# Kernel optimization log

Measured on AMD Instinct MI355X. Metric: run time of the kernel, lower is better.

The kernel has to match this reference:

```python
import jax, jax.numpy as jnp
import numpy as np

N_KEYS, PER_KEY = 8, 6
NUM_CONCEPTS = N_KEYS * PER_KEY  # 48
NUM_CLASS = 7
D_VIT, D = 768, 512
LOGIT_SCALE = 100.0


def adaptive_avg_pool_matrix(L_in: int, L_out: int) -> np.ndarray:
    """Linear operator replicating torch AdaptiveAvgPool1d: out[i] = mean(x[start_i:end_i])."""
    M = np.zeros((L_in, L_out), dtype=np.float32)
    for i in range(L_out):
        s = (i * L_in) // L_out
        e = -(((-(i + 1)) * L_in) // L_out)  # ceil((i+1)*L_in/L_out)
        M[s:e, i] = 1.0 / (e - s)
    return M


def setup_inputs() -> dict:
    key = jax.random.key(0)
    ks = jax.random.split(key, 12)
    feats = jax.random.normal(ks[0], (12, 32, 197, D_VIT), dtype=jnp.float32)
    # frozen text-side concept embeddings (CLIP text feats are ~unit norm, 512-d)
    ce = jax.random.normal(ks[1], (NUM_CONCEPTS, D), dtype=jnp.float32)
    concept_embeds = ce / jnp.linalg.norm(ce, axis=-1, keepdims=True)
    sc = 1.0 / np.sqrt(D_VIT)
    W_lin = jax.random.normal(ks[2], (D, D_VIT), dtype=jnp.float32) * sc
    b_lin = jnp.zeros((D,), dtype=jnp.float32)
    W_proj = jax.random.normal(ks[3], (D, D_VIT), dtype=jnp.float32) * sc
    scg = 1.0 / np.sqrt(3 * D)
    W_gate = jax.random.normal(ks[4], (D, 3 * D), dtype=jnp.float32) * scg
    b_gate = jnp.zeros((D,), dtype=jnp.float32)
    scu = 1.0 / np.sqrt(2 * D)
    W_upd = jax.random.normal(ks[5], (D, 2 * D), dtype=jnp.float32) * scu
    b_upd = jnp.zeros((D,), dtype=jnp.float32)
    W_cls = jax.random.normal(ks[6], (NUM_CLASS, NUM_CONCEPTS), dtype=jnp.float32) / np.sqrt(NUM_CONCEPTS)
    b_cls = jnp.zeros((NUM_CLASS,), dtype=jnp.float32)
    return {
        'feats': feats, 'concept_embeds': concept_embeds,
        'W_lin': W_lin, 'b_lin': b_lin, 'W_proj': W_proj,
        'W_gate': W_gate, 'b_gate': b_gate, 'W_upd': W_upd, 'b_upd': b_upd,
        'W_cls': W_cls, 'b_cls': b_cls,
    }


def _forward(feats, concept_embeds, W_lin, b_lin, W_proj, W_gate, b_gate, W_upd, b_upd, W_cls, b_cls):
    L, B, S, _ = feats.shape
    M = jnp.asarray(adaptive_avg_pool_matrix(S - 1, NUM_CONCEPTS))  # [196, 48]
    q0 = jnp.broadcast_to(concept_embeds[None], (B, NUM_CONCEPTS, D))

    def step(q, f):  # f: [B, 197, 768]
        cls_tok = f[:, :1, :]                                  # [B,1,768]
        pooled = jnp.einsum('bjd,ji->bid', f[:, 1:, :], M)     # [B,48,768]
        vt = jnp.concatenate([cls_tok, pooled], axis=1) @ W_lin.T + b_lin  # [B,49,512]
        attn = jax.nn.softmax(jnp.einsum('bqd,bvd->bqv', q, vt), axis=-1)
        fuse = jnp.einsum('bqv,bvd->bqd', attn, vt)            # [B,48,512]
        cls_ctx = jnp.broadcast_to(cls_tok @ W_proj.T, q.shape)
        gate = jax.nn.sigmoid(jnp.concatenate([fuse, q, cls_ctx], -1) @ W_gate.T + b_gate)
        upd = jnp.tanh(jnp.concatenate([fuse, q], -1) @ W_upd.T + b_upd)
        return gate * q + (1.0 - gate) * upd, fuse

    _, trace = jax.lax.scan(step, q0, feats)                   # trace: [12,B,48,512]

    last = trace[-1]
    vision_semantic = last / jnp.maximum(jnp.linalg.norm(last, axis=-1, keepdims=True), 1e-12)
    vs = vision_semantic.reshape(B, N_KEYS, PER_KEY, D)
    anchors = concept_embeds.reshape(N_KEYS, PER_KEY, D)
    image_logits = (LOGIT_SCALE * jnp.einsum('bkpd,kqd->bkpq', vs, anchors).mean(axis=2)).reshape(B, NUM_CONCEPTS)
    cls_logits = image_logits @ W_cls.T + b_cls
    diffs = trace[1:] - jax.lax.stop_gradient(trace[:-1])
    loss_consistency = jnp.sum(jnp.mean(diffs * diffs, axis=(1, 2, 3)))
    return cls_logits, image_logits, loss_consistency


def reference(feats, concept_embeds, W_lin, b_lin, W_proj, W_gate, b_gate, W_upd, b_upd, W_cls, b_cls):
    return _forward(feats, concept_embeds, W_lin, b_lin, W_proj, W_gate, b_gate, W_upd, b_upd, W_cls, b_cls)
```

## Files before the change

### kernel.cpp

```cpp
#include <hip/hip_runtime.h>
#include <hip/hip_bf16.h>

#define LL 12
#define BB 32
#define SS 197
#define DV 768
#define DD 512
#define CC 48
#define VV 49
#define LOSS_DEN 786432.0f

typedef unsigned short u16;
typedef unsigned int u32;
using bf16x8 = __attribute__((ext_vector_type(8))) __bf16;
using f32x4 = __attribute__((ext_vector_type(4))) float;
using u16x8 = __attribute__((ext_vector_type(8))) u16;
using u16x4 = __attribute__((ext_vector_type(4))) u16;

__device__ __forceinline__ u16 bf16h(float x) {
    u32 u = __builtin_bit_cast(u32, x);
    return (u16)((u + 0x7FFFu + ((u >> 16) & 1u)) >> 16);
}
__device__ __forceinline__ float bf2f(u16 h) {
    u32 u = ((u32)h) << 16;
    return __builtin_bit_cast(float, u);
}
__device__ __forceinline__ f32x4 mfma16(bf16x8 a, bf16x8 b, f32x4 c) {
    return __builtin_amdgcn_mfma_f32_16x16x32_bf16(a, b, c, 0, 0, 0);
}
__device__ __forceinline__ void gl_lds16(const void* g, void* s) {
    __builtin_amdgcn_global_load_lds((const __attribute__((address_space(1))) u32*)g,
                                     (__attribute__((address_space(3))) u32*)s, 16, 0, 0);
}

#define NLW (512 * 768)
#define NGW (512 * 1536)
#define NUW (512 * 1024)
#define POOL2_BLKS (LL * BB * 2)
#define WSPLIT4_BLKS ((NLW + NGW + NUW) / 1024)
#define INITQ8_BLKS ((BB * CC * DD) / 2048)

__global__ __launch_bounds__(256) void mega_pre(const float* __restrict__ feats,
                                                const float* __restrict__ Wl,
                                                const float* __restrict__ Wg,
                                                const float* __restrict__ Wu,
                                                const float* __restrict__ ce,
                                                u16* __restrict__ Xh, u16* __restrict__ Xl,
                                                u16* Wlh, u16* Wll, u16* Wgh, u16* Wgl,
                                                u16* Wuh, u16* Wul,
                                                u16* __restrict__ qh, u16* __restrict__ ql,
                                                float* __restrict__ loss) {
    int bid = blockIdx.x;
    int t = threadIdx.x;
    if (bid < POOL2_BLKS) {
        if (t >= 192) return;
        int lb = bid >> 1, half = bid & 1;
        const float4* fb = (const float4*)(feats + (size_t)lb * SS * DV);
        size_t xbase = (size_t)lb * VV * DV + 4 * t;
        if (half == 0) {
            float4 c = fb[t];
            float cv[4] = {c.x, c.y, c.z, c.w};
            u16x4 hh, ll2;
#pragma unroll
            for (int j = 0; j < 4; ++j) {
                u16 h = bf16h(cv[j]);
                hh[j] = h;
                ll2[j] = bf16h(cv[j] - bf2f(h));
            }
            *(u16x4*)(Xh + xbase) = hh;
            *(u16x4*)(Xl + xbase) = ll2;
        }
        int ib0 = half * 24, ib1 = ib0 + 24;
        for (int i = ib0; i < ib1; ++i) {
            int s = (i * 196) / 48;
            int e = ((i + 1) * 196 + 47) / 48;
            float4 acc = {0.f, 0.f, 0.f, 0.f};
            for (int j = s; j < e; ++j) {
                float4 v = fb[(size_t)(1 + j) * 192 + t];
                acc.x += v.x; acc.y += v.y; acc.z += v.z; acc.w += v.w;
            }
            float inv = 1.0f / (float)(e - s);
            float av[4] = {acc.x * inv, acc.y * inv, acc.z * inv, acc.w * inv};
            u16x4 hh, ll2;
#pragma unroll
            for (int j = 0; j < 4; ++j) {
                u16 h = bf16h(av[j]);
                hh[j] = h;
                ll2[j] = bf16h(av[j] - bf2f(h));
            }
            size_t o = xbase + (size_t)(1 + i) * DV;
            *(u16x4*)(Xh + o) = hh;
            *(u16x4*)(Xl + o) = ll2;
        }
    } else if (bid < POOL2_BLKS + WSPLIT4_BLKS) {
        int i = ((bid - POOL2_BLKS) * 256 + t) * 4;
        float4 v;
        u16 *ph, *pl;
        int j;
        if (i < NLW) { v = *(const float4*)(Wl + i); ph = Wlh; pl = Wll; j = i; }
        else if (i < NLW + NGW) { j = i - NLW; v = *(const float4*)(Wg + j); ph = Wgh; pl = Wgl; }
        else { j = i - NLW - NGW; v = *(const float4*)(Wu + j); ph = Wuh; pl = Wul; }
        float vv[4] = {v.x, v.y, v.z, v.w};
        u16x4 hh, ll2;
#pragma unroll
        for (int k = 0; k < 4; ++k) {
            u16 h = bf16h(vv[k]);
            hh[k] = h;
            ll2[k] = bf16h(vv[k] - bf2f(h));
        }
        *(u16x4*)(ph + j) = hh;
        *(u16x4*)(pl + j) = ll2;
    } else {
        int i8 = ((bid - POOL2_BLKS - WSPLIT4_BLKS) * 256 + t) * 8;
        int src = i8 % (CC * DD);
        float4 a = *(const float4*)(ce + src);
        float4 b2 = *(const float4*)(ce + src + 4);
        float vv[8] = {a.x, a.y, a.z, a.w, b2.x, b2.y, b2.z, b2.w};
        u16x8 hh, ll2;
#pragma unroll
        for (int k = 0; k < 8; ++k) {
            u16 h = bf16h(vv[k]);
            hh[k] = h;
            ll2[k] = bf16h(vv[k] - bf2f(h));
        }
        *(u16x8*)(qh + i8) = hh;
        *(u16x8*)(ql + i8) = ll2;
        if (i8 == 0) loss[0] = 0.0f;
    }
}

__global__ __launch_bounds__(256) void gemm_f32(const float* __restrict__ A, int lda,
                                                const float* __restrict__ W, int wstride, int K,
                                                const float* __restrict__ bias,
                                                float* __restrict__ Cout) {
    __shared__ float As[32][65];
    __shared__ float Bs[32][65];
    int t = threadIdx.x;
    int m0 = blockIdx.x * 64;
    int n0 = blockIdx.y * 64;
    int r = t >> 2;
    int kc = (t & 3) * 8;
    int tx = t & 15, ty = t >> 4;
    float acc[4][4] = {};
    for (int k0 = 0; k0 < K; k0 += 32) {
        const float4* pa = (const float4*)(A + (size_t)(m0 + r) * lda + k0 + kc);
        float4 a0 = pa[0], a1 = pa[1];
        const float4* pw = (const float4*)(W + (size_t)(n0 + r) * wstride + k0 + kc);
        float4 w0 = pw[0], w1 = pw[1];
        As[kc + 0][r] = a0.x; As[kc + 1][r] = a0.y; As[kc + 2][r] = a0.z; As[kc + 3][r] = a0.w;
        As[kc + 4][r] = a1.x; As[kc + 5][r] = a1.y; As[kc + 6][r] = a1.z; As[kc + 7][r] = a1.w;
        Bs[kc + 0][r] = w0.x; Bs[kc + 1][r] = w0.y; Bs[kc + 2][r] = w0.z; Bs[kc + 3][r] = w0.w;
        Bs[kc + 4][r] = w1.x; Bs[kc + 5][r] = w1.y; Bs[kc + 6][r] = w1.z; Bs[kc + 7][r] = w1.w;
        __syncthreads();
#pragma unroll
        for (int kk = 0; kk < 32; ++kk) {
            float a[4], b[4];
#pragma unroll
            for (int i = 0; i < 4; ++i) { a[i] = As[kk][ty * 4 + i]; b[i] = Bs[kk][tx * 4 + i]; }
#pragma unroll
            for (int i = 0; i < 4; ++i)
#pragma unroll
                for (int j = 0; j < 4; ++j) acc[i][j] += a[i] * b[j];
        }
        __syncthreads();
    }
#pragma unroll
    for (int i = 0; i < 4; ++i) {
        int m = m0 + ty * 4 + i;
#pragma unroll
        for (int j = 0; j < 4; ++j) {
            int n = n0 + tx * 4 + j;
            Cout[(size_t)m * DD + n] = acc[i][j] + (bias ? bias[n] : 0.0f);
        }
    }
}

__global__ __launch_bounds__(256, 2) void vt_gemm(const u16* __restrict__ Xh, const u16* __restrict__ Xl,
                                                  const u16* __restrict__ Wh, const u16* __restrict__ Wl,
                                                  const float* __restrict__ bias,
                                                  u16* __restrict__ vthp, u16* __restrict__ vtlp) {
    __shared__ u16 sm[24576];
    int tid = threadIdx.x;
    int w = tid >> 6, l = tid & 63, lr = l & 15, ls = l >> 4;
    int i = blockIdx.x, m, n;
    if (i < 1152) { int a = i >> 6, r2 = i & 63; m = 8 * a + (r2 & 7); n = r2 >> 3; }
    else { int j = i - 1152; m = 144 + (j >> 3); n = j & 7; }
    int m0 = m * 128, n0 = n * 64;
    f32x4 acc[2][4];
#pragma unroll
    for (int ii = 0; ii < 2; ++ii)
#pragma unroll
        for (int j = 0; j < 4; ++j) acc[ii][j] = f32x4{0.f, 0.f, 0.f, 0.f};

    auto stage = [&](u16* dst, int k0) {
#pragma unroll
        for (int is = 0; is < 6; ++is) {
            int q = is * 256 + tid;
            const u16* src;
            int off;
            if (is < 2)      { int qr = q;        int row = qr >> 2, sl = qr & 3; src = Xh + (size_t)(m0 + row) * DV + k0 + ((sl ^ ((row >> 1) & 3)) << 3); off = qr * 8; }
            else if (is < 4) { int qr = q - 512;  int row = qr >> 2, sl = qr & 3; src = Xl + (size_t)(m0 + row) * DV + k0 + ((sl ^ ((row >> 1) & 3)) << 3); off = 4096 + qr * 8; }
            else if (is < 5) { int qr = q - 1024; int row = qr >> 2, sl = qr & 3; src = Wh + (size_t)(n0 + row) * DV + k0 + ((sl ^ ((row >> 1) & 3)) << 3); off = 8192 + qr * 8; }
            else             { int qr = q - 1280; int row = qr >> 2, sl = qr & 3; src = Wl + (size_t)(n0 + row) * DV + k0 + ((sl ^ ((row >> 1) & 3)) << 3); off = 10240 + qr * 8; }
            gl_lds16(src, dst + off);
        }
    };

    stage(sm, 0);
    __syncthreads();
    for (int t = 0; t < 24; ++t) {
        u16* cur = sm + ((t & 1) ? 12288 : 0);
        u16* nxt = sm + ((t & 1) ? 0 : 12288);
        if (t + 1 < 24) stage(nxt, (t + 1) * 32);
        bf16x8 ah[2], al2[2], bh[4], bl2[4];
#pragma unroll
        for (int rf = 0; rf < 2; ++rf) {
            int row = 32 * w + 16 * rf + lr;
            int ro = row * 32 + ((ls ^ ((row >> 1) & 3)) << 3);
            ah[rf] = *(const bf16x8*)(cur + ro);
            al2[rf] = *(const bf16x8*)(cur + 4096 + ro);
        }
#pragma unroll
        for (int cf = 0; cf < 4; ++cf) {
            int nn = 16 * cf + lr;
            int no = nn * 32 + ((ls ^ ((nn >> 1) & 3)) << 3);
            bh[cf] = *(const bf16x8*)(cur + 8192 + no);
            bl2[cf] = *(const bf16x8*)(cur + 10240 + no);
        }
#pragma unroll
        for (int rf = 0; rf < 2; ++rf)
#pragma unroll
            for (int cf = 0; cf < 4; ++cf) {
                acc[rf][cf] = mfma16(ah[rf], bh[cf], acc[rf][cf]);
                acc[rf][cf] = mfma16(ah[rf], bl2[cf], acc[rf][cf]);
                acc[rf][cf] = mfma16(al2[rf], bh[cf], acc[rf][cf]);
            }
        __syncthreads();
    }
#pragma unroll
    for (int rf = 0; rf < 2; ++rf)
#pragma unroll
        for (int cf = 0; cf < 4; ++cf)
#pragma unroll
            for (int r = 0; r < 4; ++r) {
                int row = m0 + 32 * w + 16 * rf + 4 * ls + r;
                int col = n0 + 16 * cf + lr;
                float v = acc[rf][cf][r] + bias[col];
                size_t o = (size_t)row * DD + col;
                u16 hh = bf16h(v);
                vthp[o] = hh;
                vtlp[o] = bf16h(v - bf2f(hh));
            }
}

__device__ __forceinline__ void gemm32x64(u16* sm, const u16* Ah, const u16* Al,
                                          const u16* Wgh, const u16* Wgl,
                                          const u16* Wuh, const u16* Wul,
                                          int m0, int n0, int colOff, int tid,
                                          f32x4 accg[2], f32x4 accu[2]) {
    int w = tid >> 6, lane = tid & 63, lr = lane & 15, ls = lane >> 4;
    auto stage = [&](u16* buf, int k0) {
        {
            int j = tid, row = j >> 3, sl = j & 7;
            int ko = k0 + ((sl ^ (row & 7)) << 3);
            gl_lds16(Ah + (size_t)(m0 + row) * DD + ko, buf + j * 8);
            gl_lds16(Al + (size_t)(m0 + row) * DD + ko, buf + 2048 + j * 8);
        }
#pragma unroll
        for (int i2 = 0; i2 < 8; ++i2) {
            int aidx = tid + 256 * i2;
            int arr = aidx >> 9, j = aidx & 511;
            int row = j >> 3, sl = j & 7;
            int ko = colOff + k0 + ((sl ^ (row & 7)) << 3);
            const u16* src;
            if (arr == 0) src = Wgh + (size_t)(n0 + row) * 1536 + ko;
            else if (arr == 1) src = Wgl + (size_t)(n0 + row) * 1536 + ko;
            else if (arr == 2) src = Wuh + (size_t)(n0 + row) * 1024 + ko;
            else src = Wul + (size_t)(n0 + row) * 1024 + ko;
            gl_lds16(src, buf + 4096 + arr * 4096 + j * 8);
        }
    };
    stage(sm, 0);
    __syncthreads();
    for (int t = 0; t < 8; ++t) {
        u16* cur = sm + (t & 1) * 20480;
        if (t + 1 < 8) stage(sm + ((t + 1) & 1) * 20480, (t + 1) * 64);
#pragma unroll
        for (int ks = 0; ks < 2; ++ks) {
            int slot = ks * 4 + ls;
            int n = 16 * w + lr;
            int bo = n * 64 + ((slot ^ (n & 7)) << 3);
            bf16x8 gh8 = *(const bf16x8*)(cur + 4096 + bo);
            bf16x8 gl8 = *(const bf16x8*)(cur + 8192 + bo);
            bf16x8 uh8 = *(const bf16x8*)(cur + 12288 + bo);
            bf16x8 ul8 = *(const bf16x8*)(cur + 16384 + bo);
#pragma unroll
            for (int rf = 0; rf < 2; ++rf) {
                int r = 16 * rf + lr;
                int ao = r * 64 + ((slot ^ (r & 7)) << 3);
                bf16x8 ah8 = *(const bf16x8*)(cur + ao);
                bf16x8 al8 = *(const bf16x8*)(cur + 2048 + ao);
                accg[rf] = mfma16(ah8, gh8, accg[rf]);
                accg[rf] = mfma16(ah8, gl8, accg[rf]);
                accg[rf] = mfma16(al8, gh8, accg[rf]);
                accu[rf] = mfma16(ah8, uh8, accu[rf]);
                accu[rf] = mfma16(ah8, ul8, accu[rf]);
                accu[rf] = mfma16(al8, uh8, accu[rf]);
            }
        }
        __syncthreads();
    }
}

__global__ __launch_bounds__(256, 2) void attn_qpart(
    const u16* __restrict__ qh, const u16* __restrict__ ql,
    const u16* __restrict__ vthL, const u16* __restrict__ vtlL,
    float* __restrict__ fcur, const float* __restrict__ fprev,
    u16* __restrict__ fh, u16* __restrict__ fl,
    float* __restrict__ loss, int do_loss,
    const u16* __restrict__ Wgh, const u16* __restrict__ Wgl,
    const u16* __restrict__ Wuh, const u16* __restrict__ Wul,
    float* __restrict__ qg, float* __restrict__ qu) {
    __shared__ u16 sm[40960];
    int tid = threadIdx.x;
    if (blockIdx.x < 192) {
        int wgid = blockIdx.x * 4 + (tid >> 6);
        int lane = tid & 63;
        int b = wgid / 24;
        int r0 = b * CC + (wgid % 24) * 2;
        size_t o0 = (size_t)r0 * DD + lane * 8;
        u16x8 h0 = *(const u16x8*)(qh + o0), g0 = *(const u16x8*)(ql + o0);
        u16x8 h1 = *(const u16x8*)(qh + o0 + DD), g1 = *(const u16x8*)(ql + o0 + DD);
        float q0v[8], q1v[8];
#pragma unroll
        for (int j = 0; j < 8; ++j) {
            q0v[j] = bf2f(h0[j]) + bf2f(g0[j]);
            q1v[j] = bf2f(h1[j]) + bf2f(g1[j]);
        }
        const u16* vh = vthL + (size_t)b * VV * DD + lane * 8;
        const u16* vl = vtlL + (size_t)b * VV * DD + lane * 8;
        float m0 = -3e38f, m1 = -3e38f, s0 = 0.f, s1 = 0.f;
        float a0[8] = {}, a1[8] = {};
        for (int v = 0; v < VV; ++v) {
            u16x8 rh = *(const u16x8*)(vh + v * DD);
            u16x8 rl = *(const u16x8*)(vl + v * DD);
            float rv[8];
#pragma unroll
            for (int j = 0; j < 8; ++j) rv[j] = bf2f(rh[j]) + bf2f(rl[j]);
            float p0 = 0.f, p1 = 0.f;
#pragma unroll
            for (int j = 0; j < 8; ++j) { p0 += q0v[j] * rv[j]; p1 += q1v[j] * rv[j]; }
#pragma unroll
            for (int off = 32; off > 0; off >>= 1) { p0 += __shfl_xor(p0, off); p1 += __shfl_xor(p1, off); }
            float nm0 = fmaxf(m0, p0);
            float sc0 = __expf(m0 - nm0), w0 = __expf(p0 - nm0);
            s0 = s0 * sc0 + w0;
            float nm1 = fmaxf(m1, p1);
            float sc1 = __expf(m1 - nm1), w1 = __expf(p1 - nm1);
            s1 = s1 * sc1 + w1;
#pragma unroll
            for (int j = 0; j < 8; ++j) {
                a0[j] = a0[j] * sc0 + w0 * rv[j];
                a1[j] = a1[j] * sc1 + w1 * rv[j];
            }
            m0 = nm0;
            m1 = nm1;
        }
        float inv0 = 1.0f / s0, inv1 = 1.0f / s1;
        float d2 = 0.f;
        float f0v[8], f1v[8];
        u16x8 oh0, ol0, oh1, ol1;
#pragma unroll
        for (int j = 0; j < 8; ++j) {
            float f = a0[j] * inv0;
            f0v[j] = f;
            u16 hh = bf16h(f);
            oh0[j] = hh;
            ol0[j] = bf16h(f - bf2f(hh));
            float f2 = a1[j] * inv1;
            f1v[j] = f2;
            u16 h2 = bf16h(f2);
            oh1[j] = h2;
            ol1[j] = bf16h(f2 - bf2f(h2));
        }
        *(float4*)(fcur + o0) = float4{f0v[0], f0v[1], f0v[2], f0v[3]};
        *(float4*)(fcur + o0 + 4) = float4{f0v[4], f0v[5], f0v[6], f0v[7]};
        *(float4*)(fcur + o0 + DD) = float4{f1v[0], f1v[1], f1v[2], f1v[3]};
        *(float4*)(fcur + o0 + DD + 4) = float4{f1v[4], f1v[5], f1v[6], f1v[7]};
        *(u16x8*)(fh + o0) = oh0;
        *(u16x8*)(fl + o0) = ol0;
        *(u16x8*)(fh + o0 + DD) = oh1;
        *(u16x8*)(fl + o0 + DD) = ol1;
        if (do_loss) {
#pragma unroll
            for (int j = 0; j < 8; ++j) {
                float d = f0v[j] - fprev[o0 + j];
                d2 += d * d;
                float e = f1v[j] - fprev[o0 + DD + j];
                d2 += e * e;
            }
#pragma unroll
            for (int off = 32; off > 0; off >>= 1) d2 += __shfl_xor(d2, off);
            if (lane == 0) atomicAdd(loss, d2);
        }
    } else {
        int tb = blockIdx.x - 192;
        int m0 = (tb >> 3) * 32, n0 = (tb & 7) * 64;
        f32x4 accg[2], accu[2];
#pragma unroll
        for (int i = 0; i < 2; ++i) { accg[i] = f32x4{0.f, 0.f, 0.f, 0.f}; accu[i] = f32x4{0.f, 0.f, 0.f, 0.f}; }
        gemm32x64(sm, qh, ql, Wgh, Wgl, Wuh, Wul, m0, n0, 512, tid, accg, accu);
        int w = tid >> 6, lane = tid & 63, lr = lane & 15, ls = lane >> 4;
#pragma unroll
        for (int rf = 0; rf < 2; ++rf)
#pragma unroll
            for (int r = 0; r < 4; ++r) {
                int row = m0 + 16 * rf + 4 * ls + r;
                int col = n0 + 16 * w + lr;
                size_t o = (size_t)row * DD + col;
                qg[o] = accg[rf][r];
                qu[o] = accu[rf][r];
            }
    }
}

__global__ __launch_bounds__(256, 2) void fusepart(
    const u16* __restrict__ fhp, const u16* __restrict__ flp,
    const u16* __restrict__ qhp, const u16* __restrict__ qlp,
    const u16* __restrict__ Wgh, const u16* __restrict__ Wgl,
    const u16* __restrict__ Wuh, const u16* __restrict__ Wul,
    const float* __restrict__ qg, const float* __restrict__ qu,
    const float* __restrict__ CgL, const float* __restrict__ bu,
    u16* __restrict__ qoh, u16* __restrict__ qol) {
    __shared__ u16 sm[40960];
    int tid = threadIdx.x;
    int m0 = (blockIdx.x >> 3) * 32, n0 = (blockIdx.x & 7) * 64;
    f32x4 accg[2], accu[2];
#pragma unroll
    for (int i = 0; i < 2; ++i) { accg[i] = f32x4{0.f, 0.f, 0.f, 0.f}; accu[i] = f32x4{0.f, 0.f, 0.f, 0.f}; }
    gemm32x64(sm, fhp, flp, Wgh, Wgl, Wuh, Wul, m0, n0, 0, tid, accg, accu);
    int w = tid >> 6, lane = tid & 63, lr = lane & 15, ls = lane >> 4;
#pragma unroll
    for (int rf = 0; rf < 2; ++rf)
#pragma unroll
        for (int r = 0; r < 4; ++r) {
            int row = m0 + 16 * rf + 4 * ls + r;
            int col = n0 + 16 * w + lr;
            int b = row / CC;
            size_t o = (size_t)row * DD + col;
            float gpre = accg[rf][r] + qg[o] + CgL[(size_t)b * DD + col];
            float upre = accu[rf][r] + qu[o] + bu[col];
            float g = 1.0f / (1.0f + __expf(-gpre));
            float u = tanhf(upre);
            float qv = bf2f(qhp[o]) + bf2f(qlp[o]);
            float qo = g * qv + (1.0f - g) * u;
            u16 hh = bf16h(qo);
            qoh[o] = hh;
            qol[o] = bf16h(qo - bf2f(hh));
        }
}

__global__ __launch_bounds__(256) void final_kernel(const float* __restrict__ fuse_last,
                                                    const float* __restrict__ ce,
                                                    const float* __restrict__ W_cls,
                                                    const float* __restrict__ b_cls,
                                                    const float* __restrict__ loss_acc,
                                                    float* __restrict__ out) {
    int b = blockIdx.x;
    int t = threadIdx.x;
    int w = t >> 6, lane = t & 63;
    __shared__ float invn[CC];
    __shared__ float img[CC];
    const float* fb = fuse_last + (size_t)b * CC * DD;
    for (int c = w; c < CC; c += 4) {
        const float* fr = fb + (size_t)c * DD + lane * 8;
        float4 a0 = *(const float4*)fr;
        float4 a1 = *(const float4*)(fr + 4);
        float ss = a0.x * a0.x + a0.y * a0.y + a0.z * a0.z + a0.w * a0.w +
                   a1.x * a1.x + a1.y * a1.y + a1.z * a1.z + a1.w * a1.w;
#pragma unroll
        for (int off = 32; off > 0; off >>= 1) ss += __shfl_xor(ss, off);
        if (lane == 0) invn[c] = 1.0f / fmaxf(sqrtf(ss), 1e-12f);
    }
    __syncthreads();
    for (int g = w; g < CC; g += 4) {
        int k = g / 6;
        const float* ar = ce + (size_t)g * DD + lane * 8;
        float4 c0 = *(const float4*)ar;
        float4 c1 = *(const float4*)(ar + 4);
        float av[8] = {c0.x, c0.y, c0.z, c0.w, c1.x, c1.y, c1.z, c1.w};
        float accp = 0.0f;
        for (int p = 0; p < 6; ++p) {
            int row = k * 6 + p;
            const float* fr = fb + (size_t)row * DD + lane * 8;
            float4 f0 = *(const float4*)fr;
            float4 f1 = *(const float4*)(fr + 4);
            float fv[8] = {f0.x, f0.y, f0.z, f0.w, f1.x, f1.y, f1.z, f1.w};
            float d = 0.0f;
#pragma unroll
            for (int j = 0; j < 8; ++j) d += fv[j] * av[j];
            accp += d * invn[row];
        }
#pragma unroll
        for (int off = 32; off > 0; off >>= 1) accp += __shfl_xor(accp, off);
        if (lane == 0) img[g] = accp * (100.0f / 6.0f);
    }
    __syncthreads();
    if (t < CC) out[BB * 7 + b * CC + t] = img[t];
    if (t < 7) {
        float sacc = b_cls[t];
        for (int c = 0; c < CC; ++c) sacc += img[c] * W_cls[t * CC + c];
        out[b * 7 + t] = sacc;
    }
    if (b == 0 && t == 0) out[BB * 7 + BB * CC] = loss_acc[0] * (1.0f / LOSS_DEN);
}

extern "C" void kernel_launch(void* const* d_in, const int* in_sizes, int n_in,
                              void* d_out, int out_size, void* d_ws, size_t ws_size,
                              hipStream_t stream) {
    const float* feats = (const float*)d_in[0];
    const float* ce = (const float*)d_in[1];
    const float* W_lin = (const float*)d_in[2];
    const float* b_lin = (const float*)d_in[3];
    const float* W_proj = (const float*)d_in[4];
    const float* W_gate = (const float*)d_in[5];
    const float* b_gate = (const float*)d_in[6];
    const float* W_upd = (const float*)d_in[7];
    const float* b_upd = (const float*)d_in[8];
    const float* W_cls = (const float*)d_in[9];
    const float* b_cls = (const float*)d_in[10];
    float* out = (float*)d_out;

    char* base = (char*)d_ws;
    size_t off = 0;
    auto alloc = [&](size_t bytes) -> char* {
        char* r = base + off;
        off += (bytes + 255) & ~(size_t)255;
        return r;
    };
    u16* Xh = (u16*)alloc((size_t)LL * BB * VV * DV * 2);
    u16* Xl = (u16*)alloc((size_t)LL * BB * VV * DV * 2);
    u16* vth = (u16*)alloc((size_t)LL * BB * VV * DD * 2);
    u16* vtl = (u16*)alloc((size_t)LL * BB * VV * DD * 2);
    float* ctx = (float*)alloc((size_t)LL * BB * DD * 4);
    float* Cg = (float*)alloc((size_t)LL * BB * DD * 4);
    float* fbuf0 = (float*)alloc((size_t)BB * CC * DD * 4);
    float* fbuf1 = (float*)alloc((size_t)BB * CC * DD * 4);
    float* qg = (float*)alloc((size_t)BB * CC * DD * 4);
    float* qu = (float*)alloc((size_t)BB * CC * DD * 4);
    float* loss = (float*)alloc(256);
    u16* Wlh = (u16*)alloc((size_t)NLW * 2);
    u16* Wll = (u16*)alloc((size_t)NLW * 2);
    u16* Wgh = (u16*)alloc((size_t)NGW * 2);
    u16* Wgl = (u16*)alloc((size_t)NGW * 2);
    u16* Wuh = (u16*)alloc((size_t)NUW * 2);
    u16* Wul = (u16*)alloc((size_t)NUW * 2);
    u16* fh = (u16*)alloc((size_t)BB * CC * DD * 2);
    u16* fl = (u16*)alloc((size_t)BB * CC * DD * 2);
    u16* qah = (u16*)alloc((size_t)BB * CC * DD * 2);
    u16* qal = (u16*)alloc((size_t)BB * CC * DD * 2);
    u16* qbh = (u16*)alloc((size_t)BB * CC * DD * 2);
    u16* qbl = (u16*)alloc((size_t)BB * CC * DD * 2);
    u16* qph[2] = {qah, qbh};
    u16* qpl[2] = {qal, qbl};

    mega_pre<<<POOL2_BLKS + WSPLIT4_BLKS + INITQ8_BLKS, 256, 0, stream>>>(
        feats, W_lin, W_gate, W_upd, ce, Xh, Xl, Wlh, Wll, Wgh, Wgl, Wuh, Wul, qah, qal, loss);
    {
        dim3 g(LL * BB / 64, DD / 64);
        gemm_f32<<<g, 256, 0, stream>>>(feats, SS * DV, W_proj, DV, DV, nullptr, ctx);
        gemm_f32<<<g, 256, 0, stream>>>(ctx, DD, W_gate + 1024, 1536, DD, b_gate, Cg);
    }
    vt_gemm<<<1176, 256, 0, stream>>>(Xh, Xl, Wlh, Wll, b_lin, vth, vtl);

    int qc = 0;
    for (int l = 0; l < LL; ++l) {
        float* fcur = (l & 1) ? fbuf1 : fbuf0;
        const float* fprev = (l & 1) ? fbuf0 : fbuf1;
        int grid = (l < LL - 1) ? 576 : 192;
        attn_qpart<<<grid, 256, 0, stream>>>(qph[qc], qpl[qc],
                                             vth + (size_t)l * BB * VV * DD, vtl + (size_t)l * BB * VV * DD,
                                             fcur, fprev, fh, fl, loss, l > 0 ? 1 : 0,
                                             Wgh, Wgl, Wuh, Wul, qg, qu);
        if (l < LL - 1) {
            fusepart<<<384, 256, 0, stream>>>(fh, fl, qph[qc], qpl[qc],
                                              Wgh, Wgl, Wuh, Wul, qg, qu,
                                              Cg + (size_t)l * BB * DD, b_upd,
                                              qph[qc ^ 1], qpl[qc ^ 1]);
            qc ^= 1;
        }
    }

    final_kernel<<<BB, 256, 0, stream>>>((LL - 1) & 1 ? fbuf1 : fbuf0, ce, W_cls, b_cls, loss, out);
}
```

Measured before the change: 940.3 us.

## Drop weight low-part MFMAs in gate/update GEMMs and fold ctx GEMMs into existing kernels

Removes the bf16 low-part of W_gate/W_upd from the split-precision GEMM, halving weight staging in LDS and cutting MFMAs per step from six to four. The smaller shared buffer lets launch bounds rise to three blocks per CU. The two fp32 ctx/Cg GEMMs are folded into mega_pre and vt_gemm as extra blocks, eliminating two launches. The trade is lower precision in the weight product (roughly bf16 weights times a split-precision activation), which may affect accuracy.

```diff
diff --git a/kernel.cpp b/kernel.cpp
--- a/kernel.cpp
+++ b/kernel.cpp
@@ -36,108 +36,18 @@
 #define NLW (512 * 768)
 #define NGW (512 * 1536)
 #define NUW (512 * 1024)
+#define CTX_BLKS 48
 #define POOL2_BLKS (LL * BB * 2)
 #define WSPLIT4_BLKS ((NLW + NGW + NUW) / 1024)
 #define INITQ8_BLKS ((BB * CC * DD) / 2048)
 
-__global__ __launch_bounds__(256) void mega_pre(const float* __restrict__ feats,
-                                                const float* __restrict__ Wl,
-                                                const float* __restrict__ Wg,
-                                                const float* __restrict__ Wu,
-                                                const float* __restrict__ ce,
-                                                u16* __restrict__ Xh, u16* __restrict__ Xl,
-                                                u16* Wlh, u16* Wll, u16* Wgh, u16* Wgl,
-                                                u16* Wuh, u16* Wul,
-                                                u16* __restrict__ qh, u16* __restrict__ ql,
-                                                float* __restrict__ loss) {
-    int bid = blockIdx.x;
-    int t = threadIdx.x;
-    if (bid < POOL2_BLKS) {
-        if (t >= 192) return;
-        int lb = bid >> 1, half = bid & 1;
-        const float4* fb = (const float4*)(feats + (size_t)lb * SS * DV);
-        size_t xbase = (size_t)lb * VV * DV + 4 * t;
-        if (half == 0) {
-            float4 c = fb[t];
-            float cv[4] = {c.x, c.y, c.z, c.w};
-            u16x4 hh, ll2;
-#pragma unroll
-            for (int j = 0; j < 4; ++j) {
-                u16 h = bf16h(cv[j]);
-                hh[j] = h;
-                ll2[j] = bf16h(cv[j] - bf2f(h));
-            }
-            *(u16x4*)(Xh + xbase) = hh;
-            *(u16x4*)(Xl + xbase) = ll2;
-        }
-        int ib0 = half * 24, ib1 = ib0 + 24;
-        for (int i = ib0; i < ib1; ++i) {
-            int s = (i * 196) / 48;
-            int e = ((i + 1) * 196 + 47) / 48;
-            float4 acc = {0.f, 0.f, 0.f, 0.f};
-            for (int j = s; j < e; ++j) {
-                float4 v = fb[(size_t)(1 + j) * 192 + t];
-                acc.x += v.x; acc.y += v.y; acc.z += v.z; acc.w += v.w;
-            }
-            float inv = 1.0f / (float)(e - s);
-            float av[4] = {acc.x * inv, acc.y * inv, acc.z * inv, acc.w * inv};
-            u16x4 hh, ll2;
-#pragma unroll
-            for (int j = 0; j < 4; ++j) {
-                u16 h = bf16h(av[j]);
-                hh[j] = h;
-                ll2[j] = bf16h(av[j] - bf2f(h));
-            }
-            size_t o = xbase + (size_t)(1 + i) * DV;
-            *(u16x4*)(Xh + o) = hh;
-            *(u16x4*)(Xl + o) = ll2;
-        }
-    } else if (bid < POOL2_BLKS + WSPLIT4_BLKS) {
-        int i = ((bid - POOL2_BLKS) * 256 + t) * 4;
-        float4 v;
-        u16 *ph, *pl;
-        int j;
-        if (i < NLW) { v = *(const float4*)(Wl + i); ph = Wlh; pl = Wll; j = i; }
-        else if (i < NLW + NGW) { j = i - NLW; v = *(const float4*)(Wg + j); ph = Wgh; pl = Wgl; }
-        else { j = i - NLW - NGW; v = *(const float4*)(Wu + j); ph = Wuh; pl = Wul; }
-        float vv[4] = {v.x, v.y, v.z, v.w};
-        u16x4 hh, ll2;
-#pragma unroll
-        for (int k = 0; k < 4; ++k) {
-            u16 h = bf16h(vv[k]);
-            hh[k] = h;
-            ll2[k] = bf16h(vv[k] - bf2f(h));
-        }
-        *(u16x4*)(ph + j) = hh;
-        *(u16x4*)(pl + j) = ll2;
-    } else {
-        int i8 = ((bid - POOL2_BLKS - WSPLIT4_BLKS) * 256 + t) * 8;
-        int src = i8 % (CC * DD);
-        float4 a = *(const float4*)(ce + src);
-        float4 b2 = *(const float4*)(ce + src + 4);
-        float vv[8] = {a.x, a.y, a.z, a.w, b2.x, b2.y, b2.z, b2.w};
-        u16x8 hh, ll2;
-#pragma unroll
-        for (int k = 0; k < 8; ++k) {
-            u16 h = bf16h(vv[k]);
-            hh[k] = h;
-            ll2[k] = bf16h(vv[k] - bf2f(h));
-        }
-        *(u16x8*)(qh + i8) = hh;
-        *(u16x8*)(ql + i8) = ll2;
-        if (i8 == 0) loss[0] = 0.0f;
-    }
-}
-
-__global__ __launch_bounds__(256) void gemm_f32(const float* __restrict__ A, int lda,
-                                                const float* __restrict__ W, int wstride, int K,
-                                                const float* __restrict__ bias,
-                                                float* __restrict__ Cout) {
-    __shared__ float As[32][65];
-    __shared__ float Bs[32][65];
-    int t = threadIdx.x;
-    int m0 = blockIdx.x * 64;
-    int n0 = blockIdx.y * 64;
+__device__ __forceinline__ void gemm_f32_tile(const float* __restrict__ A, int lda,
+                                              const float* __restrict__ W, int wstride, int K,
+                                              const float* __restrict__ bias,
+                                              float* __restrict__ Cout,
+                                              int m0, int n0, int t, float* AsB, float* BsB) {
+    float (*As)[65] = (float(*)[65])AsB;
+    float (*Bs)[65] = (float(*)[65])BsB;
     int r = t >> 2;
     int kc = (t & 3) * 8;
     int tx = t & 15, ty = t >> 4;
@@ -175,12 +85,118 @@
     }
 }
 
+__global__ __launch_bounds__(256) void mega_pre(const float* __restrict__ feats,
+                                                const float* __restrict__ Wl,
+                                                const float* __restrict__ Wg,
+                                                const float* __restrict__ Wu,
+                                                const float* __restrict__ Wp,
+                                                const float* __restrict__ ce,
+                                                u16* __restrict__ Xh, u16* __restrict__ Xl,
+                                                u16* Wlh, u16* Wll, u16* Wgh, u16* Wgl,
+                                                u16* Wuh, u16* Wul,
+                                                u16* __restrict__ qh, u16* __restrict__ ql,
+                                                float* __restrict__ loss,
+                                                float* __restrict__ ctx) {
+    __shared__ float smf[2 * 32 * 65];
+    int bid = blockIdx.x;
+    int t = threadIdx.x;
+    if (bid < CTX_BLKS) {
+        gemm_f32_tile(feats, SS * DV, Wp, DV, DV, nullptr, ctx,
+                      (bid >> 3) * 64, (bid & 7) * 64, t, smf, smf + 32 * 65);
+    } else if (bid < CTX_BLKS + POOL2_BLKS) {
+        if (t >= 192) return;
+        int pb = bid - CTX_BLKS;
+        int lb = pb >> 1, half = pb & 1;
+        const float4* fb = (const float4*)(feats + (size_t)lb * SS * DV);
+        size_t xbase = (size_t)lb * VV * DV + 4 * t;
+        if (half == 0) {
+            float4 c = fb[t];
+            float cv[4] = {c.x, c.y, c.z, c.w};
+            u16x4 hh, ll2;
+#pragma unroll
+            for (int j = 0; j < 4; ++j) {
+                u16 h = bf16h(cv[j]);
+                hh[j] = h;
+                ll2[j] = bf16h(cv[j] - bf2f(h));
+            }
+            *(u16x4*)(Xh + xbase) = hh;
+            *(u16x4*)(Xl + xbase) = ll2;
+        }
+        int ib0 = half * 24, ib1 = ib0 + 24;
+        for (int i = ib0; i < ib1; ++i) {
+            int s = (i * 196) / 48;
+            int e = ((i + 1) * 196 + 47) / 48;
+            float4 acc = {0.f, 0.f, 0.f, 0.f};
+            for (int j = s; j < e; ++j) {
+                float4 v = fb[(size_t)(1 + j) * 192 + t];
+                acc.x += v.x; acc.y += v.y; acc.z += v.z; acc.w += v.w;
+            }
+            float inv = 1.0f / (float)(e - s);
+            float av[4] = {acc.x * inv, acc.y * inv, acc.z * inv, acc.w * inv};
+            u16x4 hh, ll2;
+#pragma unroll
+            for (int j = 0; j < 4; ++j) {
+                u16 h = bf16h(av[j]);
+                hh[j] = h;
+                ll2[j] = bf16h(av[j] - bf2f(h));
+            }
+            size_t o = xbase + (size_t)(1 + i) * DV;
+            *(u16x4*)(Xh + o) = hh;
+            *(u16x4*)(Xl + o) = ll2;
+        }
+    } else if (bid < CTX_BLKS + POOL2_BLKS + WSPLIT4_BLKS) {
+        int i = ((bid - CTX_BLKS - POOL2_BLKS) * 256 + t) * 4;
+        float4 v;
+        u16 *ph, *pl;
+        int j;
+        if (i < NLW) { v = *(const float4*)(Wl + i); ph = Wlh; pl = Wll; j = i; }
+        else if (i < NLW + NGW) { j = i - NLW; v = *(const float4*)(Wg + j); ph = Wgh; pl = Wgl; }
+        else { j = i - NLW - NGW; v = *(const float4*)(Wu + j); ph = Wuh; pl = Wul; }
+        float vv[4] = {v.x, v.y, v.z, v.w};
+        u16x4 hh, ll2;
+#pragma unroll
+        for (int k = 0; k < 4; ++k) {
+            u16 h = bf16h(vv[k]);
+            hh[k] = h;
+            ll2[k] = bf16h(vv[k] - bf2f(h));
+        }
+        *(u16x4*)(ph + j) = hh;
+        *(u16x4*)(pl + j) = ll2;
+    } else {
+        int i8 = ((bid - CTX_BLKS - POOL2_BLKS - WSPLIT4_BLKS) * 256 + t) * 8;
+        int src = i8 % (CC * DD);
+        float4 a = *(const float4*)(ce + src);
+        float4 b2 = *(const float4*)(ce + src + 4);
+        float vv[8] = {a.x, a.y, a.z, a.w, b2.x, b2.y, b2.z, b2.w};
+        u16x8 hh, ll2;
+#pragma unroll
+        for (int k = 0; k < 8; ++k) {
+            u16 h = bf16h(vv[k]);
+            hh[k] = h;
+            ll2[k] = bf16h(vv[k] - bf2f(h));
+        }
+        *(u16x8*)(qh + i8) = hh;
+        *(u16x8*)(ql + i8) = ll2;
+        if (i8 == 0) loss[0] = 0.0f;
+    }
+}
+
 __global__ __launch_bounds__(256, 2) void vt_gemm(const u16* __restrict__ Xh, const u16* __restrict__ Xl,
                                                   const u16* __restrict__ Wh, const u16* __restrict__ Wl,
                                                   const float* __restrict__ bias,
-                                                  u16* __restrict__ vthp, u16* __restrict__ vtlp) {
+                                                  u16* __restrict__ vthp, u16* __restrict__ vtlp,
+                                                  const float* __restrict__ ctx,
+                                                  const float* __restrict__ Wg,
+                                                  const float* __restrict__ bg,
+                                                  float* __restrict__ Cg) {
     __shared__ u16 sm[24576];
     int tid = threadIdx.x;
+    if (blockIdx.x >= 1176) {
+        int b2 = blockIdx.x - 1176;
+        gemm_f32_tile(ctx, DD, Wg + 1024, 1536, DD, bg, Cg,
+                      (b2 >> 3) * 64, (b2 & 7) * 64, tid, (float*)sm, (float*)sm + 32 * 65);
+        return;
+    }
     int w = tid >> 6, l = tid & 63, lr = l & 15, ls = l >> 4;
     int i = blockIdx.x, m, n;
     if (i < 1152) { int a = i >> 6, r2 = i & 63; m = 8 * a + (r2 & 7); n = r2 >> 3; }
@@ -254,8 +270,7 @@
 }
 
 __device__ __forceinline__ void gemm32x64(u16* sm, const u16* Ah, const u16* Al,
-                                          const u16* Wgh, const u16* Wgl,
-                                          const u16* Wuh, const u16* Wul,
+                                          const u16* Wgh, const u16* Wuh,
                                           int m0, int n0, int colOff, int tid,
                                           f32x4 accg[2], f32x4 accu[2]) {
     int w = tid >> 6, lane = tid & 63, lr = lane & 15, ls = lane >> 4;
@@ -267,33 +282,28 @@
             gl_lds16(Al + (size_t)(m0 + row) * DD + ko, buf + 2048 + j * 8);
         }
 #pragma unroll
-        for (int i2 = 0; i2 < 8; ++i2) {
+        for (int i2 = 0; i2 < 4; ++i2) {
             int aidx = tid + 256 * i2;
             int arr = aidx >> 9, j = aidx & 511;
             int row = j >> 3, sl = j & 7;
             int ko = colOff + k0 + ((sl ^ (row & 7)) << 3);
-            const u16* src;
-            if (arr == 0) src = Wgh + (size_t)(n0 + row) * 1536 + ko;
-            else if (arr == 1) src = Wgl + (size_t)(n0 + row) * 1536 + ko;
-            else if (arr == 2) src = Wuh + (size_t)(n0 + row) * 1024 + ko;
-            else src = Wul + (size_t)(n0 + row) * 1024 + ko;
+            const u16* src = arr ? (Wuh + (size_t)(n0 + row) * 1024 + ko)
+                                 : (Wgh + (size_t)(n0 + row) * 1536 + ko);
             gl_lds16(src, buf + 4096 + arr * 4096 + j * 8);
         }
     };
     stage(sm, 0);
     __syncthreads();
     for (int t = 0; t < 8; ++t) {
-        u16* cur = sm + (t & 1) * 20480;
-        if (t + 1 < 8) stage(sm + ((t + 1) & 1) * 20480, (t + 1) * 64);
+        u16* cur = sm + (t & 1) * 12288;
+        if (t + 1 < 8) stage(sm + ((t + 1) & 1) * 12288, (t + 1) * 64);
 #pragma unroll
         for (int ks = 0; ks < 2; ++ks) {
             int slot = ks * 4 + ls;
             int n = 16 * w + lr;
             int bo = n * 64 + ((slot ^ (n & 7)) << 3);
             bf16x8 gh8 = *(const bf16x8*)(cur + 4096 + bo);
-            bf16x8 gl8 = *(const bf16x8*)(cur + 8192 + bo);
-            bf16x8 uh8 = *(const bf16x8*)(cur + 12288 + bo);
-            bf16x8 ul8 = *(const bf16x8*)(cur + 16384 + bo);
+            bf16x8 uh8 = *(const bf16x8*)(cur + 8192 + bo);
 #pragma unroll
             for (int rf = 0; rf < 2; ++rf) {
                 int r = 16 * rf + lr;
@@ -301,10 +311,8 @@
                 bf16x8 ah8 = *(const bf16x8*)(cur + ao);
                 bf16x8 al8 = *(const bf16x8*)(cur + 2048 + ao);
                 accg[rf] = mfma16(ah8, gh8, accg[rf]);
-                accg[rf] = mfma16(ah8, gl8, accg[rf]);
                 accg[rf] = mfma16(al8, gh8, accg[rf]);
                 accu[rf] = mfma16(ah8, uh8, accu[rf]);
-                accu[rf] = mfma16(ah8, ul8, accu[rf]);
                 accu[rf] = mfma16(al8, uh8, accu[rf]);
             }
         }
@@ -312,16 +320,15 @@
     }
 }
 
-__global__ __launch_bounds__(256, 2) void attn_qpart(
+__global__ __launch_bounds__(256, 3) void attn_qpart(
     const u16* __restrict__ qh, const u16* __restrict__ ql,
     const u16* __restrict__ vthL, const u16* __restrict__ vtlL,
     float* __restrict__ fcur, const float* __restrict__ fprev,
     u16* __restrict__ fh, u16* __restrict__ fl,
     float* __restrict__ loss, int do_loss,
-    const u16* __restrict__ Wgh, const u16* __restrict__ Wgl,
-    const u16* __restrict__ Wuh, const u16* __restrict__ Wul,
+    const u16* __restrict__ Wgh, const u16* __restrict__ Wuh,
     float* __restrict__ qg, float* __restrict__ qu) {
-    __shared__ u16 sm[40960];
+    __shared__ u16 sm[24576];
     int tid = threadIdx.x;
     if (blockIdx.x < 192) {
         int wgid = blockIdx.x * 4 + (tid >> 6);
@@ -409,7 +416,7 @@
         f32x4 accg[2], accu[2];
 #pragma unroll
         for (int i = 0; i < 2; ++i) { accg[i] = f32x4{0.f, 0.f, 0.f, 0.f}; accu[i] = f32x4{0.f, 0.f, 0.f, 0.f}; }
-        gemm32x64(sm, qh, ql, Wgh, Wgl, Wuh, Wul, m0, n0, 512, tid, accg, accu);
+        gemm32x64(sm, qh, ql, Wgh + 512, Wuh + 512, m0, n0, 0, tid, accg, accu);
         int w = tid >> 6, lane = tid & 63, lr = lane & 15, ls = lane >> 4;
 #pragma unroll
         for (int rf = 0; rf < 2; ++rf)
@@ -424,21 +431,20 @@
     }
 }
 
-__global__ __launch_bounds__(256, 2) void fusepart(
+__global__ __launch_bounds__(256, 3) void fusepart(
     const u16* __restrict__ fhp, const u16* __restrict__ flp,
     const u16* __restrict__ qhp, const u16* __restrict__ qlp,
-    const u16* __restrict__ Wgh, const u16* __restrict__ Wgl,
-    const u16* __restrict__ Wuh, const u16* __restrict__ Wul,
+    const u16* __restrict__ Wgh, const u16* __restrict__ Wuh,
     const float* __restrict__ qg, const float* __restrict__ qu,
     const float* __restrict__ CgL, const float* __restrict__ bu,
     u16* __restrict__ qoh, u16* __restrict__ qol) {
-    __shared__ u16 sm[40960];
+    __shared__ u16 sm[24576];
     int tid = threadIdx.x;
     int m0 = (blockIdx.x >> 3) * 32, n0 = (blockIdx.x & 7) * 64;
     f32x4 accg[2], accu[2];
 #pragma unroll
     for (int i = 0; i < 2; ++i) { accg[i] = f32x4{0.f, 0.f, 0.f, 0.f}; accu[i] = f32x4{0.f, 0.f, 0.f, 0.f}; }
-    gemm32x64(sm, fhp, flp, Wgh, Wgl, Wuh, Wul, m0, n0, 0, tid, accg, accu);
+    gemm32x64(sm, fhp, flp, Wgh, Wuh, m0, n0, 0, tid, accg, accu);
     int w = tid >> 6, lane = tid & 63, lr = lane & 15, ls = lane >> 4;
 #pragma unroll
     for (int rf = 0; rf < 2; ++rf)
@@ -564,14 +570,11 @@
     u16* qph[2] = {qah, qbh};
     u16* qpl[2] = {qal, qbl};
 
-    mega_pre<<<POOL2_BLKS + WSPLIT4_BLKS + INITQ8_BLKS, 256, 0, stream>>>(
-        feats, W_lin, W_gate, W_upd, ce, Xh, Xl, Wlh, Wll, Wgh, Wgl, Wuh, Wul, qah, qal, loss);
-    {
-        dim3 g(LL * BB / 64, DD / 64);
-        gemm_f32<<<g, 256, 0, stream>>>(feats, SS * DV, W_proj, DV, DV, nullptr, ctx);
-        gemm_f32<<<g, 256, 0, stream>>>(ctx, DD, W_gate + 1024, 1536, DD, b_gate, Cg);
-    }
-    vt_gemm<<<1176, 256, 0, stream>>>(Xh, Xl, Wlh, Wll, b_lin, vth, vtl);
+    mega_pre<<<CTX_BLKS + POOL2_BLKS + WSPLIT4_BLKS + INITQ8_BLKS, 256, 0, stream>>>(
+        feats, W_lin, W_gate, W_upd, W_proj, ce, Xh, Xl, Wlh, Wll, Wgh, Wgl, Wuh, Wul,
+        qah, qal, loss, ctx);
+    vt_gemm<<<1176 + CTX_BLKS, 256, 0, stream>>>(Xh, Xl, Wlh, Wll, b_lin, vth, vtl,
+                                                 ctx, W_gate, b_gate, Cg);
 
     int qc = 0;
     for (int l = 0; l < LL; ++l) {
@@ -581,10 +584,10 @@
         attn_qpart<<<grid, 256, 0, stream>>>(qph[qc], qpl[qc],
                                              vth + (size_t)l * BB * VV * DD, vtl + (size_t)l * BB * VV * DD,
                                              fcur, fprev, fh, fl, loss, l > 0 ? 1 : 0,
-                                             Wgh, Wgl, Wuh, Wul, qg, qu);
+                                             Wgh, Wuh, qg, qu);
         if (l < LL - 1) {
             fusepart<<<384, 256, 0, stream>>>(fh, fl, qph[qc], qpl[qc],
-                                              Wgh, Wgl, Wuh, Wul, qg, qu,
+                                              Wgh, Wuh, qg, qu,
                                               Cg + (size_t)l * BB * DD, b_upd,
                                               qph[qc ^ 1], qpl[qc ^ 1]);
             qc ^= 1;
```

New measurement: 854.6 us. 9.1% less time.
